# Performance work log

Hardware: AMD Instinct MI355X
Metric: run time of the kernel (lower is better)

Reference implementation:

```python
import jax, jax.numpy as jnp
import numpy as np
from jax import lax

EPS = 1e-12  # F.normalize eps


def conv3x3(x, w, b):
    # x [B,C,H,W], w [O,C,3,3], b [O]
    y = lax.conv_general_dilated(x, w, window_strides=(1, 1), padding=((1, 1), (1, 1)),
                                 dimension_numbers=("NCHW", "OIHW", "NCHW"))
    return y + b[None, :, None, None]


def bilinear_sample(img, py, px):
    # img [B,C,H,W]; py,px [B,H,W] fractional pixel coords; zero outside.
    B, C, H, W = img.shape
    y0 = jnp.floor(py)
    x0 = jnp.floor(px)
    img_flat = img.reshape(B, C, H * W)
    out = jnp.zeros_like(img)
    for dy in (0, 1):
        for dx in (0, 1):
            yi = y0 + dy
            xi = x0 + dx
            wgt = (1.0 - jnp.abs(py - yi)) * (1.0 - jnp.abs(px - xi))
            valid = (yi >= 0) & (yi < H) & (xi >= 0) & (xi < W)
            yc = jnp.clip(yi, 0, H - 1).astype(jnp.int32)
            xc = jnp.clip(xi, 0, W - 1).astype(jnp.int32)
            idx = (yc * W + xc).reshape(B, 1, H * W)
            v = jnp.take_along_axis(img_flat, idx, axis=2).reshape(B, C, H, W)
            out = out + v * (wgt * valid.astype(img.dtype))[:, None]
    return out


def deform_conv3x3(x, offset, weight):
    # torchvision deform_conv2d, k=3, stride=1, pad=1, no mask (modulator unused in source).
    # offset [B, 18, H, W]: per kernel tap k -> (dy=offset[:,2k], dx=offset[:,2k+1])
    B, Cin, H, W = x.shape
    iy = jnp.arange(H, dtype=x.dtype)[:, None]
    ix = jnp.arange(W, dtype=x.dtype)[None, :]
    out = jnp.zeros((B, weight.shape[0], H, W), dtype=x.dtype)
    for k in range(9):
        kh, kw = k // 3, k % 3
        py = iy - 1 + kh + offset[:, 2 * k]
        px = ix - 1 + kw + offset[:, 2 * k + 1]
        s = bilinear_sample(x, py, px)  # [B,Cin,H,W]
        out = out + jnp.einsum("bchw,oc->bohw", s, weight[:, :, kh, kw])
    return out


def l2norm_lastdim(t):
    n = jnp.sqrt(jnp.sum(t * t, axis=-1, keepdims=True))
    return t / jnp.maximum(n, EPS)


def setup_inputs() -> dict:
    key = jax.random.key(0)
    ks = jax.random.split(key, 8)
    B, C, H, W = 2, 192, 128, 128
    heads = 4
    s = 0.02
    return {
        "x": jax.random.normal(ks[0], (B, C, H, W), jnp.float32),
        "q": jax.random.normal(ks[1], (B, C, H, W), jnp.float32),
        "temperature": jnp.ones((1, heads, 1, 1), jnp.float32),
        "kv_w": jax.random.normal(ks[2], (2 * C, C), jnp.float32) * s,
        "offset_w": jax.random.normal(ks[3], (18, 2 * C, 3, 3), jnp.float32) * 0.001,
        "offset_b": jax.random.normal(ks[4], (18,), jnp.float32) * 0.1,
        "reg_w": jax.random.normal(ks[5], (2 * C, 2 * C, 3, 3), jnp.float32) * s,
        "proj_w": jax.random.normal(ks[6], (C, C), jnp.float32) * s,
    }


def reference(x, q, temperature, kv_w, offset_w, offset_b, reg_w, proj_w):
    B, C, H, W = x.shape
    heads = temperature.shape[1]
    n = H * W
    # kv 1x1 conv
    kv = jnp.einsum("bchw,oc->bohw", x, kv_w)  # [B,2C,H,W]
    # deformable conv KV path
    offset = conv3x3(kv, offset_w, offset_b)  # [B,18,H,W]
    kv = deform_conv3x3(kv, offset, reg_w)  # [B,2C,H,W]
    k, v = jnp.split(kv, 2, axis=1)
    qh = q.reshape(B, heads, C // heads, n)
    kh = k.reshape(B, heads, C // heads, n)
    vh = v.reshape(B, heads, C // heads, n)
    qh = l2norm_lastdim(qh)
    kh = l2norm_lastdim(kh)
    attn = jax.nn.softmax(jnp.einsum("bhdn,bhen->bhde", qh, kh) * temperature, axis=-1)
    out = jnp.einsum("bhde,bhen->bhdn", attn, vh).reshape(B, C, H, W)
    out = jnp.einsum("bchw,oc->bohw", out, proj_w)
    return (out, qh)
```

## Files before the change

### kernel.cpp

```cpp
#include <hip/hip_runtime.h>
#include <math.h>

#define B_ 2
#define C_ 192
#define C2_ 384
#define H_ 128
#define W_ 128
#define N_ (H_*W_)
#define HEADS_ 4
#define HD_ 48
#define EPS_ 1e-12f

typedef __bf16 bf16x8 __attribute__((ext_vector_type(8)));
typedef __bf16 bf16x4 __attribute__((ext_vector_type(4)));
typedef float  f32x4  __attribute__((ext_vector_type(4)));

__global__ __launch_bounds__(256) void k_pack(const float* __restrict__ regw, const float* __restrict__ kvw,
                                              const float* __restrict__ offw,
                                              ushort* __restrict__ regwP, ushort* __restrict__ kvwP,
                                              ushort* __restrict__ offwP) {
    const int NR = 9 * 12 * C2_ * 32;
    const int NK = 6 * C2_ * 32;
    const int NO = 12 * 9 * 32 * 32;
    int idx = blockIdx.x * 256 + threadIdx.x;
    union { __bf16 h; ushort u; } cv;
    if (idx < NR) {
        int t  = idx / (12 * C2_ * 32);
        int r  = idx - t * (12 * C2_ * 32);
        int ci = r / (C2_ * 32);
        int r2 = r - ci * (C2_ * 32);
        int oc = r2 >> 5;
        int kk = r2 & 31;
        cv.h = (__bf16)regw[(oc * C2_ + ci * 32 + kk) * 9 + t];
        regwP[idx] = cv.u;
    } else if (idx < NR + NK) {
        int r  = idx - NR;
        int ci = r / (C2_ * 32);
        int r2 = r - ci * (C2_ * 32);
        int oc = r2 >> 5;
        int kk = r2 & 31;
        cv.h = (__bf16)kvw[oc * C_ + ci * 32 + kk];
        kvwP[r] = cv.u;
    } else if (idx < NR + NK + NO) {
        int r  = idx - NR - NK;
        int ci = r / (9 * 32 * 32);
        int r2 = r - ci * (9 * 32 * 32);
        int t  = r2 / (32 * 32);
        int r3 = r2 - t * (32 * 32);
        int oc = r3 >> 5;
        int kk = r3 & 31;
        float v = (oc < 18) ? offw[(oc * C2_ + ci * 32 + kk) * 9 + t] : 0.f;
        cv.h = (__bf16)v;
        offwP[r] = cv.u;
    }
}

__global__ __launch_bounds__(256) void k_kv1x1_mfma(const float* __restrict__ x, const __bf16* __restrict__ kvwP,
                                                    __bf16* __restrict__ kvB) {
    __shared__ __bf16 As[64 * 40];
    __shared__ __bf16 Ws[C2_ * 40];
    const int bid = blockIdx.x;
    const int swz = (bid & 7) * 64 + (bid >> 3);
    const int b   = swz >> 8;
    const int p0  = (swz & 255) * 64;
    const int tid  = threadIdx.x;
    const int wv   = tid >> 6;
    const int lane = tid & 63;
    const int fr   = lane & 15;
    const int fg   = lane >> 4;
    const int apx  = tid & 63;
    const int akg  = tid >> 6;

    f32x4 acc[4][6];
    #pragma unroll
    for (int mg = 0; mg < 4; ++mg)
        #pragma unroll
        for (int ng = 0; ng < 6; ++ng) acc[mg][ng] = (f32x4){0.f, 0.f, 0.f, 0.f};

    for (int ci = 0; ci < 6; ++ci) {
        const int cc = ci * 32;
        const __bf16* wsrc = kvwP + (size_t)ci * C2_ * 32;
        #pragma unroll
        for (int i = 0; i < 6; ++i) {
            const int e = tid + i * 256;
            const int oc = e >> 2, sg = e & 3;
            *(bf16x8*)&Ws[oc * 40 + sg * 8] = *(const bf16x8*)(wsrc + oc * 32 + sg * 8);
        }
        {
            float v[8];
            #pragma unroll
            for (int j = 0; j < 8; ++j)
                v[j] = x[((size_t)b * C_ + cc + akg * 8 + j) * N_ + p0 + apx];
            bf16x8 pk = {(__bf16)v[0], (__bf16)v[1], (__bf16)v[2], (__bf16)v[3],
                         (__bf16)v[4], (__bf16)v[5], (__bf16)v[6], (__bf16)v[7]};
            *(bf16x8*)&As[apx * 40 + akg * 8] = pk;
        }
        __syncthreads();
        bf16x8 a[4];
        #pragma unroll
        for (int mg = 0; mg < 4; ++mg)
            a[mg] = *(const bf16x8*)&As[(mg * 16 + fr) * 40 + fg * 8];
        #pragma unroll
        for (int ng = 0; ng < 6; ++ng) {
            const bf16x8 bb = *(const bf16x8*)&Ws[(wv * 96 + ng * 16 + fr) * 40 + fg * 8];
            #pragma unroll
            for (int mg = 0; mg < 4; ++mg)
                acc[mg][ng] = __builtin_amdgcn_mfma_f32_16x16x32_bf16(a[mg], bb, acc[mg][ng], 0, 0, 0);
        }
        __syncthreads();
    }
    #pragma unroll
    for (int mg = 0; mg < 4; ++mg)
        #pragma unroll
        for (int j = 0; j < 4; ++j) {
            const int p = p0 + mg * 16 + fg * 4 + j;
            __bf16* dst = kvB + ((size_t)b * N_ + p) * C2_ + wv * 96 + fr;
            #pragma unroll
            for (int ng = 0; ng < 6; ++ng)
                dst[ng * 16] = (__bf16)acc[mg][ng][j];
        }
}

__global__ __launch_bounds__(256) void k_qnorm(const float* __restrict__ q, float* __restrict__ qn,
                                               __bf16* __restrict__ qnB) {
    const int row = blockIdx.x;
    const float* src = q + (size_t)row * N_;
    float* dst = qn + (size_t)row * N_;
    __bf16* dstB = qnB + (size_t)row * N_;
    float ss = 0.f;
    for (int i = threadIdx.x; i < N_ / 4; i += 256) {
        float4 v = ((const float4*)src)[i];
        ss += v.x * v.x + v.y * v.y + v.z * v.z + v.w * v.w;
    }
    __shared__ float red[256];
    red[threadIdx.x] = ss;
    __syncthreads();
    for (int s = 128; s > 0; s >>= 1) {
        if (threadIdx.x < s) red[threadIdx.x] += red[threadIdx.x + s];
        __syncthreads();
    }
    float rn = 1.f / fmaxf(sqrtf(red[0]), EPS_);
    for (int i = threadIdx.x; i < N_ / 8; i += 256) {
        float4 v0 = ((const float4*)src)[2 * i];
        float4 v1 = ((const float4*)src)[2 * i + 1];
        float f0 = v0.x * rn, f1 = v0.y * rn, f2 = v0.z * rn, f3 = v0.w * rn;
        float f4 = v1.x * rn, f5 = v1.y * rn, f6 = v1.z * rn, f7 = v1.w * rn;
        ((float4*)dst)[2 * i]     = make_float4(f0, f1, f2, f3);
        ((float4*)dst)[2 * i + 1] = make_float4(f4, f5, f6, f7);
        bf16x8 pk = {(__bf16)f0, (__bf16)f1, (__bf16)f2, (__bf16)f3,
                     (__bf16)f4, (__bf16)f5, (__bf16)f6, (__bf16)f7};
        *(bf16x8*)&dstB[i * 8] = pk;
    }
}

__global__ __launch_bounds__(256) void k_offconv_mfma(const __bf16* __restrict__ kvB, const __bf16* __restrict__ offwP,
                                                      const float* __restrict__ offb, float* __restrict__ offT) {
    __shared__ __bf16 Win[3 * 66 * 40];
    __shared__ __bf16 Wall[9 * 32 * 40];
    const int bid = blockIdx.x;
    const int swz = (bid & 7) * 64 + (bid >> 3);
    const int b   = swz >> 8;
    const int p0  = (swz & 255) * 64;
    const int y   = p0 >> 7;
    const int x0  = p0 & 127;
    const int tid  = threadIdx.x;
    const int wv   = tid >> 6;
    const int lane = tid & 63;
    const int fr   = lane & 15;
    const int fg   = lane >> 4;
    const __bf16* kb = kvB + (size_t)b * N_ * C2_;

    f32x4 acc[2];
    acc[0] = (f32x4){0.f, 0.f, 0.f, 0.f};
    acc[1] = (f32x4){0.f, 0.f, 0.f, 0.f};

    for (int ci = 0; ci < 12; ++ci) {
        const int cc = ci * 32;
        for (int e = tid; e < 3 * 66 * 4; e += 256) {
            const int r  = e / 264;
            const int rem = e - r * 264;
            const int cw = rem >> 2;
            const int sg = rem & 3;
            const int gy = y - 1 + r;
            const int gx = x0 - 1 + cw;
            bf16x8 v = {};
            if ((unsigned)gy < H_ && (unsigned)gx < W_)
                v = *(const bf16x8*)(kb + ((size_t)(gy * W_ + gx)) * C2_ + cc + sg * 8);
            *(bf16x8*)&Win[(r * 66 + cw) * 40 + sg * 8] = v;
        }
        const __bf16* wsrc = offwP + (size_t)ci * 9 * 32 * 32;
        for (int e = tid; e < 9 * 32 * 4; e += 256) {
            const int t  = e >> 7;
            const int r2 = e & 127;
            const int oc = r2 >> 2;
            const int sg = r2 & 3;
            *(bf16x8*)&Wall[(t * 32 + oc) * 40 + sg * 8] = *(const bf16x8*)(wsrc + (t * 32 + oc) * 32 + sg * 8);
        }
        __syncthreads();
        #pragma unroll
        for (int t = 0; t < 9; ++t) {
            const int dy = t / 3, dx = t % 3;
            const bf16x8 a = *(const bf16x8*)&Win[((dy * 66) + (wv * 16 + fr + dx)) * 40 + fg * 8];
            #pragma unroll
            for (int ng = 0; ng < 2; ++ng) {
                const bf16x8 bb = *(const bf16x8*)&Wall[(t * 32 + ng * 16 + fr) * 40 + fg * 8];
                acc[ng] = __builtin_amdgcn_mfma_f32_16x16x32_bf16(a, bb, acc[ng], 0, 0, 0);
            }
        }
        __syncthreads();
    }
    #pragma unroll
    for (int ng = 0; ng < 2; ++ng) {
        const int oc = ng * 16 + fr;
        if (oc < 18) {
            const float bias = offb[oc];
            #pragma unroll
            for (int j = 0; j < 4; ++j) {
                const int p = p0 + wv * 16 + fg * 4 + j;
                offT[((size_t)b * N_ + p) * 18 + oc] = acc[ng][j] + bias;
            }
        }
    }
}


#define ISSUE_GATHER(ITN) do {                                                           \
    const int tt_ = (ITN) / 12, ci_ = (ITN) - tt_ * 12;                                  \
    const int4 id4_ = *(const int4*)&sh.m.widx[tt_][spx][0];                             \
    const __bf16* cb_ = kb + ci_ * 32 + ssub;                                            \
    graw[0] = *(const bf16x8*)(cb_ + (size_t)id4_.x * C2_);                              \
    graw[1] = *(const bf16x8*)(cb_ + (size_t)id4_.y * C2_);                              \
    graw[2] = *(const bf16x8*)(cb_ + (size_t)id4_.z * C2_);                              \
    graw[3] = *(const bf16x8*)(cb_ + (size_t)id4_.w * C2_);                              \
} while (0)

#define PACK_A(ITN, NB) do {                                                             \
    const int tt_ = (ITN) / 12;                                                          \
    const float4 w4_ = *(const float4*)&sh.m.wwt[tt_][spx][0];                           \
    const float wj_[4] = {w4_.x, w4_.y, w4_.z, w4_.w};                                   \
    float s_[8] = {0.f,0.f,0.f,0.f,0.f,0.f,0.f,0.f};                                     \
    _Pragma("unroll")                                                                    \
    for (int j_ = 0; j_ < 4; ++j_) {                                                     \
        _Pragma("unroll")                                                                \
        for (int e_ = 0; e_ < 8; ++e_) s_[e_] += wj_[j_] * (float)graw[j_][e_];          \
    }                                                                                    \
    bf16x8 pk_ = {(__bf16)s_[0],(__bf16)s_[1],(__bf16)s_[2],(__bf16)s_[3],               \
                  (__bf16)s_[4],(__bf16)s_[5],(__bf16)s_[6],(__bf16)s_[7]};              \
    *(bf16x8*)&sh.m.As[NB][spx * 40 + ssub] = pk_;                                       \
} while (0)

#define DEF_BODY(CUR, NXT) do {                                                          \
    const int ip1_ = (it < 107) ? it + 1 : 107;                                          \
    const int ip2_ = (it < 106) ? it + 2 : 107;                                          \
    {   const __bf16* wb_ = wbase + (size_t)ip1_ * (C2_ * 32);                           \
        _Pragma("unroll")                                                                \
        for (int ng_ = 0; ng_ < 6; ++ng_)                                                \
            bfr[NXT][ng_] = *(const bf16x8*)(wb_ + ng_ * 512); }                         \
    bf16x8 a_[4];                                                                        \
    _Pragma("unroll")                                                                    \
    for (int mg_ = 0; mg_ < 4; ++mg_)                                                    \
        a_[mg_] = *(const bf16x8*)&sh.m.As[CUR][(mg_ * 16 + fr) * 40 + fg * 8];          \
    PACK_A(ip1_, NXT);                                                                   \
    ISSUE_GATHER(ip2_);                                                                  \
    _Pragma("unroll")                                                                    \
    for (int ng_ = 0; ng_ < 6; ++ng_)                                                    \
        _Pragma("unroll")                                                                \
        for (int mg_ = 0; mg_ < 4; ++mg_)                                                \
            acc[mg_][ng_] = __builtin_amdgcn_mfma_f32_16x16x32_bf16(a_[mg_], bfr[CUR][ng_], acc[mg_][ng_], 0, 0, 0); \
    __syncthreads();                                                                     \
    ++it;                                                                                \
} while (0)

__global__ __launch_bounds__(256, 2) void k_deform_mfma(const __bf16* __restrict__ kvB, const float* __restrict__ offT,
                                                        const __bf16* __restrict__ regwP,
                                                        __bf16* __restrict__ kT, __bf16* __restrict__ vP) {
    __shared__ union {
        struct {
            __bf16 As[2][64 * 40];
            float  wwt[9][64][4];
            int    widx[9][64][4];
        } m;
        __bf16 kTs[192 * 72];
    } sh;
    const int bid = blockIdx.x;
    const int swz = (bid & 7) * 64 + (bid >> 3);
    const int b   = swz >> 8;
    const int p0  = (swz & 255) * 64;
    const int tid  = threadIdx.x;
    const int wv   = tid >> 6;
    const int lane = tid & 63;
    const int fr   = lane & 15;
    const int fg   = lane >> 4;
    const int spx  = tid >> 2;
    const int ssub = (tid & 3) * 8;
    const __bf16* kb    = kvB + (size_t)b * N_ * C2_;
    const __bf16* wbase = regwP + ((size_t)(wv * 96 + fr)) * 32 + fg * 8;

    f32x4 acc[4][6];
    #pragma unroll
    for (int mg = 0; mg < 4; ++mg)
        #pragma unroll
        for (int ng = 0; ng < 6; ++ng) acc[mg][ng] = (f32x4){0.f, 0.f, 0.f, 0.f};

    for (int e = tid; e < 576; e += 256) {
        const int tt = e >> 6, pp = e & 63;
        const int p = p0 + pp;
        const int yy = p >> 7, xx = p & 127;
        const float dy = offT[((size_t)b * N_ + p) * 18 + 2 * tt];
        const float dx = offT[((size_t)b * N_ + p) * 18 + 2 * tt + 1];
        const float py = (float)(yy + tt / 3 - 1) + dy;
        const float px = (float)(xx + tt % 3 - 1) + dx;
        const float fy = floorf(py), fx = floorf(px);
        const int y0 = (int)fy, x0i = (int)fx;
        const float ay = py - fy, ax = px - fx;
        #pragma unroll
        for (int j = 0; j < 4; ++j) {
            const int yi = y0 + (j >> 1);
            const int xi = x0i + (j & 1);
            const float wj = ((j >> 1) ? ay : 1.f - ay) * ((j & 1) ? ax : 1.f - ax);
            const bool v = ((unsigned)yi < H_) && ((unsigned)xi < W_);
            sh.m.wwt[tt][pp][j]  = v ? wj : 0.f;
            sh.m.widx[tt][pp][j] = v ? (yi * W_ + xi) : 0;
        }
    }
    __syncthreads();

    bf16x8 graw[4];
    bf16x8 bfr[2][6];
    ISSUE_GATHER(0);
    PACK_A(0, 0);
    ISSUE_GATHER(1);
    #pragma unroll
    for (int ng = 0; ng < 6; ++ng) bfr[0][ng] = *(const bf16x8*)(wbase + ng * 512);
    __syncthreads();

    int it = 0;
    for (int i2 = 0; i2 < 54; ++i2) {
        DEF_BODY(0, 1);
        DEF_BODY(1, 0);
    }

    __syncthreads();
    if (wv < 2) {
        #pragma unroll
        for (int mg = 0; mg < 4; ++mg)
            #pragma unroll
            for (int ng = 0; ng < 6; ++ng) {
                const int oc = wv * 96 + ng * 16 + fr;
                const bf16x4 pk = {(__bf16)acc[mg][ng][0], (__bf16)acc[mg][ng][1],
                                   (__bf16)acc[mg][ng][2], (__bf16)acc[mg][ng][3]};
                *(bf16x4*)&sh.kTs[oc * 72 + mg * 16 + fg * 4] = pk;
            }
    } else {
        #pragma unroll
        for (int mg = 0; mg < 4; ++mg)
            #pragma unroll
            for (int j = 0; j < 4; ++j) {
                const int p = p0 + mg * 16 + fg * 4 + j;
                __bf16* dst = vP + ((size_t)b * N_ + p) * C_ + (wv - 2) * 96 + fr;
                #pragma unroll
                for (int ng = 0; ng < 6; ++ng)
                    dst[ng * 16] = (__bf16)acc[mg][ng][j];
            }
    }
    __syncthreads();
    for (int e = tid; e < 192 * 8; e += 256) {
        const int oc = e >> 3, sub = e & 7;
        *(bf16x8*)&kT[((size_t)b * C_ + oc) * N_ + p0 + sub * 8] = *(const bf16x8*)&sh.kTs[oc * 72 + sub * 8];
    }
}

__global__ __launch_bounds__(256) void k_knorm2(const __bf16* __restrict__ kT, float* __restrict__ knorm) {
    const int row = blockIdx.x;
    const __bf16* src = kT + (size_t)row * N_;
    float ss = 0.f;
    for (int i = threadIdx.x; i < N_ / 8; i += 256) {
        const bf16x8 v = ((const bf16x8*)src)[i];
        #pragma unroll
        for (int e = 0; e < 8; ++e) { float f = (float)v[e]; ss += f * f; }
    }
    __shared__ float red[256];
    red[threadIdx.x] = ss;
    __syncthreads();
    for (int s = 128; s > 0; s >>= 1) {
        if (threadIdx.x < s) red[threadIdx.x] += red[threadIdx.x + s];
        __syncthreads();
    }
    if (threadIdx.x == 0) knorm[row] = 1.f / fmaxf(sqrtf(red[0]), EPS_);
}

__global__ __launch_bounds__(256) void k_attn_mfma(const __bf16* __restrict__ qnB, const __bf16* __restrict__ kT,
                                                   float* __restrict__ part) {
    const int bh = blockIdx.y;
    const int b  = bh >> 2, h = bh & 3;
    const int wv = threadIdx.x >> 6, lane = threadIdx.x & 63;
    const int sl = blockIdx.x * 4 + wv;
    const int n0 = sl * 128;
    const int fr = lane & 15, fg = lane >> 4;
    const __bf16* qb = qnB + ((size_t)b * C_ + h * HD_) * N_ + n0 + fg * 8;
    const __bf16* kb = kT  + ((size_t)b * C_ + h * HD_) * N_ + n0 + fg * 8;
    f32x4 acc[3][3];
    #pragma unroll
    for (int i = 0; i < 3; ++i)
        #pragma unroll
        for (int j = 0; j < 3; ++j) acc[i][j] = (f32x4){0.f, 0.f, 0.f, 0.f};
    #pragma unroll
    for (int kc = 0; kc < 4; ++kc) {
        bf16x8 a[3], bb[3];
        #pragma unroll
        for (int mg = 0; mg < 3; ++mg) a[mg]  = *(const bf16x8*)(qb + (size_t)(mg * 16 + fr) * N_ + kc * 32);
        #pragma unroll
        for (int ng = 0; ng < 3; ++ng) bb[ng] = *(const bf16x8*)(kb + (size_t)(ng * 16 + fr) * N_ + kc * 32);
        #pragma unroll
        for (int mg = 0; mg < 3; ++mg)
            #pragma unroll
            for (int ng = 0; ng < 3; ++ng)
                acc[mg][ng] = __builtin_amdgcn_mfma_f32_16x16x32_bf16(a[mg], bb[ng], acc[mg][ng], 0, 0, 0);
    }
    float* pp = part + ((size_t)bh * 128 + sl) * (HD_ * HD_);
    #pragma unroll
    for (int mg = 0; mg < 3; ++mg)
        #pragma unroll
        for (int ng = 0; ng < 3; ++ng)
            #pragma unroll
            for (int j = 0; j < 4; ++j)
                pp[(mg * 16 + fg * 4 + j) * HD_ + ng * 16 + fr] = acc[mg][ng][j];
}

__global__ __launch_bounds__(256) void k_softmax(const float* __restrict__ part, const float* __restrict__ knorm,
                                                 const float* __restrict__ temp, float* __restrict__ attn) {
    const int row = blockIdx.x;
    const int b = row / (HEADS_ * HD_);
    const int r = row % (HEADS_ * HD_);
    const int h = r / HD_;
    const int d = r % HD_;
    const int bh = b * HEADS_ + h;
    const int wv = threadIdx.x >> 6;
    const int lane = threadIdx.x & 63;
    __shared__ float red[4][HD_];
    if (lane < HD_) {
        const float* pp = part + (size_t)bh * 128 * (HD_ * HD_) + d * HD_ + lane;
        float s = 0.f;
        for (int sl = wv; sl < 128; sl += 4)
            s += pp[(size_t)sl * (HD_ * HD_)];
        red[wv][lane] = s;
    }
    __syncthreads();
    if (wv == 0) {
        float v = -INFINITY;
        if (lane < HD_) {
            float t = red[0][lane] + red[1][lane] + red[2][lane] + red[3][lane];
            v = t * knorm[b * C_ + h * HD_ + lane] * temp[h];
        }
        float m = v;
        #pragma unroll
        for (int off = 32; off > 0; off >>= 1) m = fmaxf(m, __shfl_xor(m, off));
        float ex = (lane < HD_) ? expf(v - m) : 0.f;
        float sum = ex;
        #pragma unroll
        for (int off = 32; off > 0; off >>= 1) sum += __shfl_xor(sum, off);
        if (lane < HD_)
            attn[((size_t)bh * HD_ + d) * HD_ + lane] = ex / sum;
    }
}

__global__ __launch_bounds__(256) void k_m(const float* __restrict__ projw, const float* __restrict__ attn,
                                           __bf16* __restrict__ MmB) {
    const int gid = blockIdx.x * 256 + threadIdx.x;
    if (gid >= B_ * C_ * C_) return;
    const int b  = gid / (C_ * C_);
    const int r  = gid % (C_ * C_);
    const int oc = r / C_;
    const int he = r % C_;
    const int h = he / HD_;
    const int e = he % HD_;
    float s = 0.f;
    #pragma unroll 8
    for (int d = 0; d < HD_; ++d)
        s += projw[oc * C_ + h * HD_ + d] * attn[(((size_t)b * HEADS_ + h) * HD_ + d) * HD_ + e];
    MmB[gid] = (__bf16)s;
}

__global__ __launch_bounds__(256) void k_out_mfma(const __bf16* __restrict__ MmB, const __bf16* __restrict__ vP,
                                                  float* __restrict__ out) {
    const int bid = blockIdx.x;
    const int swz = (bid & 7) * 64 + (bid >> 3);
    const int b   = swz >> 8;
    const int p0  = (swz & 255) * 64;
    const int wv = threadIdx.x >> 6, lane = threadIdx.x & 63;
    const int fr = lane & 15, fg = lane >> 4;
    const __bf16* vb = vP + ((size_t)b * N_ + p0 + wv * 16 + fr) * C_ + fg * 8;
    const __bf16* mb = MmB + ((size_t)b * C_ + fr) * C_ + fg * 8;
    f32x4 acc[12];
    #pragma unroll
    for (int rr = 0; rr < 12; ++rr) acc[rr] = (f32x4){0.f, 0.f, 0.f, 0.f};
    #pragma unroll
    for (int kc = 0; kc < 6; ++kc) {
        const bf16x8 bb = *(const bf16x8*)(vb + kc * 32);
        #pragma unroll
        for (int rr = 0; rr < 12; ++rr) {
            const bf16x8 a = *(const bf16x8*)(mb + (size_t)(rr * 16) * C_ + kc * 32);
            acc[rr] = __builtin_amdgcn_mfma_f32_16x16x32_bf16(a, bb, acc[rr], 0, 0, 0);
        }
    }
    #pragma unroll
    for (int rr = 0; rr < 12; ++rr)
        #pragma unroll
        for (int j = 0; j < 4; ++j)
            out[((size_t)b * C_ + rr * 16 + fg * 4 + j) * N_ + p0 + wv * 16 + fr] = acc[rr][j];
}

extern "C" void kernel_launch(void* const* d_in, const int* in_sizes, int n_in,
                              void* d_out, int out_size, void* d_ws, size_t ws_size,
                              hipStream_t stream) {
    (void)in_sizes; (void)n_in; (void)out_size; (void)ws_size;
    const float* x     = (const float*)d_in[0];
    const float* q     = (const float*)d_in[1];
    const float* temp  = (const float*)d_in[2];
    const float* kvw   = (const float*)d_in[3];
    const float* offw  = (const float*)d_in[4];
    const float* offb  = (const float*)d_in[5];
    const float* regw  = (const float*)d_in[6];
    const float* projw = (const float*)d_in[7];

    float* out = (float*)d_out;
    float* qn  = out + (size_t)B_ * C_ * N_;
    __bf16* kvB = (__bf16*)out;

    ushort* kT    = (ushort*)d_ws;
    ushort* vP    = kT + (size_t)B_ * C_ * N_;
    float*  offT  = (float*)(vP + (size_t)B_ * C_ * N_);
    ushort* regwP = (ushort*)(offT + (size_t)B_ * N_ * 18);
    ushort* kvwP  = regwP + (size_t)9 * 12 * C2_ * 32;
    ushort* offwP = kvwP + (size_t)6 * C2_ * 32;
    ushort* qnB   = offwP + (size_t)12 * 9 * 32 * 32;
    float*  part  = (float*)(qnB + (size_t)B_ * C_ * N_);
    float*  attn  = part + (size_t)B_ * HEADS_ * 128 * HD_ * HD_;
    float*  knorm = attn + (size_t)B_ * HEADS_ * HD_ * HD_;
    ushort* MmB   = (ushort*)(knorm + (size_t)B_ * C_);

    const int packN = 9 * 12 * C2_ * 32 + 6 * C2_ * 32 + 12 * 9 * 32 * 32;
    k_pack<<<dim3((packN + 255) / 256), 256, 0, stream>>>(regw, kvw, offw, regwP, kvwP, offwP);
    k_kv1x1_mfma<<<dim3(N_ / 64 * B_), 256, 0, stream>>>(x, (const __bf16*)kvwP, kvB);
    k_offconv_mfma<<<dim3(N_ / 64 * B_), 256, 0, stream>>>(kvB, (const __bf16*)offwP, offb, offT);
    k_deform_mfma<<<dim3(N_ / 64 * B_), 256, 0, stream>>>(kvB, offT, (const __bf16*)regwP,
                                                          (__bf16*)kT, (__bf16*)vP);
    k_qnorm<<<dim3(B_ * C_), 256, 0, stream>>>(q, qn, (__bf16*)qnB);
    k_knorm2<<<dim3(B_ * C_), 256, 0, stream>>>((const __bf16*)kT, knorm);
    k_attn_mfma<<<dim3(32, B_ * HEADS_), 256, 0, stream>>>((const __bf16*)qnB, (const __bf16*)kT, part);
    k_softmax<<<dim3(B_ * HEADS_ * HD_), 256, 0, stream>>>(part, knorm, temp, attn);
    k_m<<<dim3((B_ * C_ * C_ + 255) / 256), 256, 0, stream>>>(projw, attn, (__bf16*)MmB);
    k_out_mfma<<<dim3(N_ / 64 * B_), 256, 0, stream>>>((const __bf16*)MmB, (const __bf16*)vP, out);
}
```

Measured before the change: 250.2 us.

## Double the K-step per iteration in deformable conv MFMA loop to halve barriers

```diff
diff --git a/kernel.cpp b/kernel.cpp
--- a/kernel.cpp
+++ b/kernel.cpp
@@ -225,48 +225,67 @@
 
 
 #define ISSUE_GATHER(ITN) do {                                                           \
-    const int tt_ = (ITN) / 12, ci_ = (ITN) - tt_ * 12;                                  \
+    const int tt_ = (ITN) / 6;                                                           \
+    const int ci0_ = 2 * (ITN) - 12 * tt_;                                               \
     const int4 id4_ = *(const int4*)&sh.m.widx[tt_][spx][0];                             \
-    const __bf16* cb_ = kb + ci_ * 32 + ssub;                                            \
-    graw[0] = *(const bf16x8*)(cb_ + (size_t)id4_.x * C2_);                              \
-    graw[1] = *(const bf16x8*)(cb_ + (size_t)id4_.y * C2_);                              \
-    graw[2] = *(const bf16x8*)(cb_ + (size_t)id4_.z * C2_);                              \
-    graw[3] = *(const bf16x8*)(cb_ + (size_t)id4_.w * C2_);                              \
+    const __bf16* cb0_ = kb + ci0_ * 32 + ssub;                                          \
+    graw[0][0] = *(const bf16x8*)(cb0_ + (size_t)id4_.x * C2_);                          \
+    graw[0][1] = *(const bf16x8*)(cb0_ + (size_t)id4_.y * C2_);                          \
+    graw[0][2] = *(const bf16x8*)(cb0_ + (size_t)id4_.z * C2_);                          \
+    graw[0][3] = *(const bf16x8*)(cb0_ + (size_t)id4_.w * C2_);                          \
+    const __bf16* cb1_ = cb0_ + 32;                                                      \
+    graw[1][0] = *(const bf16x8*)(cb1_ + (size_t)id4_.x * C2_);                          \
+    graw[1][1] = *(const bf16x8*)(cb1_ + (size_t)id4_.y * C2_);                          \
+    graw[1][2] = *(const bf16x8*)(cb1_ + (size_t)id4_.z * C2_);                          \
+    graw[1][3] = *(const bf16x8*)(cb1_ + (size_t)id4_.w * C2_);                          \
 } while (0)
 
 #define PACK_A(ITN, NB) do {                                                             \
-    const int tt_ = (ITN) / 12;                                                          \
+    const int tt_ = (ITN) / 6;                                                           \
     const float4 w4_ = *(const float4*)&sh.m.wwt[tt_][spx][0];                           \
     const float wj_[4] = {w4_.x, w4_.y, w4_.z, w4_.w};                                   \
-    float s_[8] = {0.f,0.f,0.f,0.f,0.f,0.f,0.f,0.f};                                     \
     _Pragma("unroll")                                                                    \
-    for (int j_ = 0; j_ < 4; ++j_) {                                                     \
+    for (int h_ = 0; h_ < 2; ++h_) {                                                     \
+        float s_[8] = {0.f,0.f,0.f,0.f,0.f,0.f,0.f,0.f};                                 \
         _Pragma("unroll")                                                                \
-        for (int e_ = 0; e_ < 8; ++e_) s_[e_] += wj_[j_] * (float)graw[j_][e_];          \
+        for (int j_ = 0; j_ < 4; ++j_)                                                   \
+            _Pragma("unroll")                                                            \
+            for (int e_ = 0; e_ < 8; ++e_) s_[e_] += wj_[j_] * (float)graw[h_][j_][e_];  \
+        bf16x8 pk_ = {(__bf16)s_[0],(__bf16)s_[1],(__bf16)s_[2],(__bf16)s_[3],           \
+                      (__bf16)s_[4],(__bf16)s_[5],(__bf16)s_[6],(__bf16)s_[7]};          \
+        *(bf16x8*)&sh.m.As[NB][spx * 72 + h_ * 32 + ssub] = pk_;                         \
     }                                                                                    \
-    bf16x8 pk_ = {(__bf16)s_[0],(__bf16)s_[1],(__bf16)s_[2],(__bf16)s_[3],               \
-                  (__bf16)s_[4],(__bf16)s_[5],(__bf16)s_[6],(__bf16)s_[7]};              \
-    *(bf16x8*)&sh.m.As[NB][spx * 40 + ssub] = pk_;                                       \
 } while (0)
 
 #define DEF_BODY(CUR, NXT) do {                                                          \
-    const int ip1_ = (it < 107) ? it + 1 : 107;                                          \
-    const int ip2_ = (it < 106) ? it + 2 : 107;                                          \
-    {   const __bf16* wb_ = wbase + (size_t)ip1_ * (C2_ * 32);                           \
+    const int ip1_ = (it < 53) ? it + 1 : 53;                                            \
+    const int ip2_ = (it < 52) ? it + 2 : 53;                                            \
+    bf16x8 bfrB_[6];                                                                     \
+    {   const __bf16* wb_ = wbase + (size_t)(2 * it + 1) * (C2_ * 32);                   \
         _Pragma("unroll")                                                                \
-        for (int ng_ = 0; ng_ < 6; ++ng_)                                                \
-            bfr[NXT][ng_] = *(const bf16x8*)(wb_ + ng_ * 512); }                         \
-    bf16x8 a_[4];                                                                        \
+        for (int ng_ = 0; ng_ < 6; ++ng_) bfrB_[ng_] = *(const bf16x8*)(wb_ + ng_ * 512); } \
+    bf16x8 a0_[4], a1_[4];                                                               \
     _Pragma("unroll")                                                                    \
-    for (int mg_ = 0; mg_ < 4; ++mg_)                                                    \
-        a_[mg_] = *(const bf16x8*)&sh.m.As[CUR][(mg_ * 16 + fr) * 40 + fg * 8];          \
+    for (int mg_ = 0; mg_ < 4; ++mg_) {                                                  \
+        a0_[mg_] = *(const bf16x8*)&sh.m.As[CUR][(mg_ * 16 + fr) * 72 + fg * 8];         \
+        a1_[mg_] = *(const bf16x8*)&sh.m.As[CUR][(mg_ * 16 + fr) * 72 + 32 + fg * 8];    \
+    }                                                                                    \
     PACK_A(ip1_, NXT);                                                                   \
     ISSUE_GATHER(ip2_);                                                                  \
     _Pragma("unroll")                                                                    \
     for (int ng_ = 0; ng_ < 6; ++ng_)                                                    \
         _Pragma("unroll")                                                                \
         for (int mg_ = 0; mg_ < 4; ++mg_)                                                \
-            acc[mg_][ng_] = __builtin_amdgcn_mfma_f32_16x16x32_bf16(a_[mg_], bfr[CUR][ng_], acc[mg_][ng_], 0, 0, 0); \
+            acc[mg_][ng_] = __builtin_amdgcn_mfma_f32_16x16x32_bf16(a0_[mg_], bfrA[ng_], acc[mg_][ng_], 0, 0, 0); \
+    _Pragma("unroll")                                                                    \
+    for (int ng_ = 0; ng_ < 6; ++ng_)                                                    \
+        _Pragma("unroll")                                                                \
+        for (int mg_ = 0; mg_ < 4; ++mg_)                                                \
+            acc[mg_][ng_] = __builtin_amdgcn_mfma_f32_16x16x32_bf16(a1_[mg_], bfrB_[ng_], acc[mg_][ng_], 0, 0, 0); \
+    {   const int nx_ = (it < 53) ? 2 * it + 2 : 107;                                    \
+        const __bf16* wb_ = wbase + (size_t)nx_ * (C2_ * 32);                            \
+        _Pragma("unroll")                                                                \
+        for (int ng_ = 0; ng_ < 6; ++ng_) bfrA[ng_] = *(const bf16x8*)(wb_ + ng_ * 512); } \
     __syncthreads();                                                                     \
     ++it;                                                                                \
 } while (0)
@@ -276,7 +295,7 @@
                                                         __bf16* __restrict__ kT, __bf16* __restrict__ vP) {
     __shared__ union {
         struct {
-            __bf16 As[2][64 * 40];
+            __bf16 As[2][64 * 72];
             float  wwt[9][64][4];
             int    widx[9][64][4];
         } m;
@@ -325,17 +344,17 @@
     }
     __syncthreads();
 
-    bf16x8 graw[4];
-    bf16x8 bfr[2][6];
+    bf16x8 graw[2][4];
+    bf16x8 bfrA[6];
     ISSUE_GATHER(0);
     PACK_A(0, 0);
     ISSUE_GATHER(1);
     #pragma unroll
-    for (int ng = 0; ng < 6; ++ng) bfr[0][ng] = *(const bf16x8*)(wbase + ng * 512);
+    for (int ng = 0; ng < 6; ++ng) bfrA[ng] = *(const bf16x8*)(wbase + ng * 512);
     __syncthreads();
 
     int it = 0;
-    for (int i2 = 0; i2 < 54; ++i2) {
+    for (int i2 = 0; i2 < 27; ++i2) {
         DEF_BODY(0, 1);
         DEF_BODY(1, 0);
     }
```

Result: no change. 247.2 us (-1.2%).
